# Optimization experiments

Hardware: AMD Instinct MI355X
Metric: run time of the kernel (lower is better)

## Reference

```python
import jax, jax.numpy as jnp
import numpy as np

B, T, DU, DM, DA, DF = 8, 2048, 512, 512, 256, 12
L_STAGES = 4   # number of routing stages
R_ITERS = 1    # diversity refinement iterations in selector
GAMMA = 1.0    # coverage_gamma
EPS = 1e-6
SCALE = float(np.sqrt(DA))


def setup_inputs() -> dict:
    key = jax.random.key(0)
    ks = jax.random.split(key, 16)
    w = lambda k, shape, fan_in: (jax.random.normal(k, shape, jnp.float32) / np.sqrt(fan_in)).astype(jnp.float32)
    return {
        'u': jax.random.normal(ks[0], (B, T, DU), jnp.float32),
        'structural_features': jax.random.normal(ks[1], (B, T, DF), jnp.float32),
        'similarity': jax.random.uniform(ks[2], (B, T, T), jnp.float32),
        'memory0': jax.random.normal(ks[3], (B, DM), jnp.float32),
        'Wq': w(ks[4], (DA, DM), DM),
        'Wk': w(ks[5], (DA, DU), DU),
        'Wv': w(ks[6], (DU, DU), DU),
        'sb_w1': w(ks[7], (DA, 3), 3),
        'sb_b1': jnp.zeros((DA,), jnp.float32),
        'sb_w2': w(ks[8], (1, DA), DA),
        'sb_b2': jnp.zeros((1,), jnp.float32),
        'log_temp': jnp.zeros((), jnp.float32),
        'W_ih': w(ks[9], (3 * DM, DU + 4), DU + 4),
        'b_ih': jnp.zeros((3 * DM,), jnp.float32),
        'W_hh': w(ks[10], (3 * DM, DM), DM),
        'b_hh': jnp.zeros((3 * DM,), jnp.float32),
    }


def _selection_stats(y, u):
    # y: [B,T], u: [B,T,DU] -> c: [B,4]
    Tn = u.shape[1]
    y_sum = jnp.maximum(y.sum(axis=1), EPS)                      # [B]
    coverage = y.sum(axis=1) / Tn
    y_norm = y / y_sum[:, None]
    entropy = -(y_norm * jnp.log(jnp.maximum(y_norm, EPS))).sum(axis=1)
    centroid = jnp.einsum('bt,btd->bd', y, u)                    # unnormalized [B,DU]
    cen = centroid / y_sum[:, None]
    dist = jnp.linalg.norm(u - cen[:, None, :], axis=-1)         # [B,T]
    spread = (y * dist).sum(axis=1) / y_sum
    wsq = (y * jnp.sum(u * u, axis=-1)).sum(axis=1)              # [B]
    csq = jnp.sum(centroid * centroid, axis=1)
    compact = 2.0 * (y_sum * wsq - csq) / jnp.maximum(y_sum * y_sum, EPS)
    return jnp.stack([coverage, entropy, spread, compact], axis=1)


def reference(u, structural_features, similarity, memory0, Wq, Wk, Wv,
              sb_w1, sb_b1, sb_w2, sb_b2, log_temp, W_ih, b_ih, W_hh, b_hh):
    k = jnp.einsum('btu,au->bta', u, Wk)                         # [B,T,DA]
    v = jnp.einsum('btu,vu->btv', u, Wv)                         # [B,T,DU]
    desc = structural_features[..., -4:-1]                       # [B,T,3]
    sbias = (jax.nn.gelu(desc @ sb_w1.T + sb_b1, approximate=False) @ sb_w2.T + sb_b2)[..., 0]
    temp = jnp.clip(jnp.exp(log_temp), 0.1, 10.0)
    memory = memory0
    prev = None
    outs = []
    for _ in range(L_STAGES):
        q = memory @ Wq.T                                        # [B,DA]
        scores = jnp.einsum('bta,ba->bt', k, q) / SCALE + sbias
        if prev is not None:
            scores = scores - GAMMA * jnp.einsum('bts,bs->bt', similarity, prev)
        logits = scores / temp
        y = jax.nn.softmax(logits, axis=1)
        for _r in range(R_ITERS):
            overlap = jnp.einsum('bts,bs->bt', similarity, y)
            penalty = overlap / jnp.maximum(jnp.max(overlap, axis=1, keepdims=True), EPS)
            logits = logits - penalty
            y = jax.nn.softmax(logits, axis=1)
        z = jnp.einsum('bt,btd->bd', y, v)                       # stage token [B,DU]
        c = _selection_stats(y, u)                               # [B,4]
        x = jnp.concatenate([z, c], axis=-1)
        gi = x @ W_ih.T + b_ih
        gh = memory @ W_hh.T + b_hh
        gir, giz, gin = jnp.split(gi, 3, axis=-1)
        ghr, ghz, ghn = jnp.split(gh, 3, axis=-1)
        rg = jax.nn.sigmoid(gir + ghr)
        zg = jax.nn.sigmoid(giz + ghz)
        ng = jnp.tanh(gin + rg * ghn)
        memory = (1.0 - zg) * ng + zg * memory                   # GRUCell update
        prev = y if prev is None else prev + y
        outs.append(z)
    return jnp.stack(outs, axis=1)                               # [B,L,DU]
```

## Files before the change

### kernel.cpp

```cpp
#include <hip/hip_runtime.h>
#include <math.h>

constexpr int cB = 8, cT = 2048, cDU = 512, cDM = 512, cDA = 256, cDF = 12, cL = 4;
constexpr float cEPS = 1e-6f;
constexpr float cSCALE = 16.0f;
constexpr float cGAMMA = 1.0f;

typedef unsigned short u16;
typedef unsigned char u8;
typedef u16 u16x8 __attribute__((ext_vector_type(8)));

constexpr size_t F_SB = 0;
constexpr size_t F_UN = F_SB + 16384;
constexpr size_t F_LG = F_UN + 16384;
constexpr size_t F_Y  = F_LG + 16384;
constexpr size_t F_PR = F_Y  + 16384;
constexpr size_t F_OV = F_PR + 16384;
constexpr size_t F_SP = F_OV + 16384;
constexpr size_t F_QK = F_SP + 256;
constexpr size_t F_M0 = F_QK + 4096;
constexpr size_t F_M1 = F_M0 + 4096;
constexpr size_t F_C  = F_M1 + 4096;
constexpr size_t F_Z  = F_C  + 4096;
constexpr size_t F_SC = F_Z  + 4096;
constexpr size_t F_END = F_SC + 64;
constexpr size_t U_OFFB   = F_END * 4;
constexpr size_t U_BYTES  = (size_t)cB * cT * cDU * 2;
constexpr size_t S8_OFFB  = U_OFFB + U_BYTES;
constexpr size_t S8_BYTES = (size_t)cB * cT * cT;
constexpr size_t WS_NEED_U   = S8_OFFB;
constexpr size_t WS_NEED_ALL = S8_OFFB + S8_BYTES;

__device__ __forceinline__ float wave_sum(float v) {
#pragma unroll
  for (int o = 32; o; o >>= 1) v += __shfl_down(v, o);
  return v;
}
__device__ __forceinline__ u16 f2bf(float f) {
  unsigned u = __float_as_uint(f);
  return (u16)((u + 0x7fffu + ((u >> 16) & 1u)) >> 16);
}
__device__ __forceinline__ float bf2f(u16 h) { return __uint_as_float(((unsigned)h) << 16); }
__device__ __forceinline__ float dot4(float4 a, float4 b) {
  return a.x * b.x + a.y * b.y + a.z * b.z + a.w * b.w;
}
__device__ __forceinline__ unsigned pack4(float a, float b, float c, float d) {
  unsigned b0 = (unsigned)(a * 255.f + 0.5f);
  unsigned b1 = (unsigned)(b * 255.f + 0.5f);
  unsigned b2 = (unsigned)(c * 255.f + 0.5f);
  unsigned b3 = (unsigned)(d * 255.f + 0.5f);
  return b0 | (b1 << 8) | (b2 << 16) | (b3 << 24);
}
__device__ __forceinline__ void dotu8(float& sd, unsigned w, float4 p) {
  sd += (float)(w & 255u) * p.x + (float)((w >> 8) & 255u) * p.y +
        (float)((w >> 16) & 255u) * p.z + (float)(w >> 24) * p.w;
}

__global__ __launch_bounds__(256) void k_init(
    const float* __restrict__ u, const float* __restrict__ sf,
    const float* __restrict__ mem0,
    const float* __restrict__ w1, const float* __restrict__ b1,
    const float* __restrict__ w2, const float* __restrict__ b2,
    float* __restrict__ wsf, u16* __restrict__ ubf, int use_ubf) {
  const int tid = threadIdx.x;
  const int gt = blockIdx.x * 256 + tid;
  const int nt = gridDim.x * 256;
  const int wv = tid >> 6, lane = tid & 63;
  const int gw = blockIdx.x * 4 + wv;
  const int nw = gridDim.x * 4;

  for (int i = gt; i < cB * cDM; i += nt) wsf[F_M0 + i] = mem0[i];

  if (use_ubf) {
    const int NU8 = cB * cT * cDU / 8;
    const float4* src = (const float4*)u;
    for (int c = gt; c < NU8; c += nt) {
      float4 f0 = src[(size_t)c * 2], f1 = src[(size_t)c * 2 + 1];
      u16x8 o;
      o[0] = f2bf(f0.x); o[1] = f2bf(f0.y); o[2] = f2bf(f0.z); o[3] = f2bf(f0.w);
      o[4] = f2bf(f1.x); o[5] = f2bf(f1.y); o[6] = f2bf(f1.z); o[7] = f2bf(f1.w);
      *(u16x8*)(ubf + (size_t)c * 8) = o;
    }
  }
  for (int row = gw; row < cB * cT; row += nw) {
    float d0 = sf[(size_t)row * cDF + 8];
    float d1 = sf[(size_t)row * cDF + 9];
    float d2 = sf[(size_t)row * cDF + 10];
    float acc = 0.f;
#pragma unroll
    for (int i = 0; i < 4; ++i) {
      int a = lane * 4 + i;
      float h = d0 * w1[a * 3 + 0] + d1 * w1[a * 3 + 1] + d2 * w1[a * 3 + 2] + b1[a];
      float g = 0.5f * h * (1.0f + erff(h * 0.70710678118654752f));
      acc += g * w2[a];
    }
    float un = 0.f;
    const float4* ur = (const float4*)(u + (size_t)row * cDU);
#pragma unroll
    for (int m = 0; m < 2; ++m) { float4 x = ur[lane + m * 64]; un += dot4(x, x); }
    acc = wave_sum(acc);
    un = wave_sum(un);
    if (lane == 0) { wsf[F_SB + row] = acc + b2[0]; wsf[F_UN + row] = un; }
  }
}

__global__ __launch_bounds__(1024) void k_qqk(const float* __restrict__ mem,
                                              const float* __restrict__ Wq,
                                              const float* __restrict__ Wk,
                                              float* __restrict__ qk,
                                              float* __restrict__ c_raw) {
  __shared__ float qs[cDA];
  __shared__ float red2[1024];
  int b = blockIdx.x, tid = threadIdx.x;
  int wv = tid >> 6, lane = tid & 63;
  if (tid < cDU) c_raw[b * cDU + tid] = 0.f;
  const float4* mr = (const float4*)(mem + (size_t)b * cDM);
  float4 m0 = mr[lane * 2], m1 = mr[lane * 2 + 1];
#pragma unroll
  for (int ii = 0; ii < 16; ++ii) {
    int a = wv * 16 + ii;
    const float4* wr = (const float4*)(Wq + (size_t)a * cDM);
    float acc = dot4(m0, wr[lane * 2]) + dot4(m1, wr[lane * 2 + 1]);
    acc = wave_sum(acc);
    if (lane == 0) qs[a] = acc;
  }
  __syncthreads();
  int j = tid & 511;
  int half = tid >> 9;
  float acc = 0.f;
#pragma unroll 4
  for (int a = half * 128; a < half * 128 + 128; ++a)
    acc += Wk[(size_t)a * cDU + j] * qs[a];
  red2[tid] = acc;
  __syncthreads();
  if (tid < 512) qk[b * cDU + j] = red2[tid] + red2[tid + 512];
}

__global__ __launch_bounds__(256) void k_scores(
    const u16* __restrict__ ubf, const float* __restrict__ uf,
    const float* __restrict__ qk, const float* __restrict__ sbias,
    const u8* __restrict__ sim8, const float* __restrict__ simf,
    const float* __restrict__ prev, const float* __restrict__ log_temp,
    float gamma, int use_ubf, int use_s8, float* __restrict__ logits) {
  int wid = (blockIdx.x * blockDim.x + threadIdx.x) >> 6;
  int lane = threadIdx.x & 63;
  int b = wid >> 11;
  const float4* qk4 = (const float4*)(qk + (size_t)b * cDU);
  float4 q0 = qk4[lane * 2], q1 = qk4[lane * 2 + 1];
  float acc;
  if (use_ubf) {
    u16x8 s = *(const u16x8*)(ubf + (size_t)wid * cDU + lane * 8);
    acc = bf2f(s[0]) * q0.x + bf2f(s[1]) * q0.y + bf2f(s[2]) * q0.z + bf2f(s[3]) * q0.w +
          bf2f(s[4]) * q1.x + bf2f(s[5]) * q1.y + bf2f(s[6]) * q1.z + bf2f(s[7]) * q1.w;
  } else {
    const float4* ur = (const float4*)(uf + (size_t)wid * cDU);
    acc = dot4(ur[lane * 2], q0) + dot4(ur[lane * 2 + 1], q1);
  }
  acc *= (1.0f / cSCALE);
  if (gamma != 0.0f) {
    float sd = 0.f;
    const float4* pr4 = (const float4*)(prev + (size_t)b * cT);
    if (use_s8) {
#pragma unroll
      for (int m = 0; m < 2; ++m) {
        uint4 sq = *(const uint4*)(sim8 + (size_t)wid * cT + m * 1024 + lane * 16);
        const float4* pb = pr4 + m * 256 + lane * 4;
        dotu8(sd, sq.x, pb[0]); dotu8(sd, sq.y, pb[1]);
        dotu8(sd, sq.z, pb[2]); dotu8(sd, sq.w, pb[3]);
      }
      sd *= (1.0f / 255.0f);
    } else {
      const float4* sr = (const float4*)(simf + (size_t)wid * cT);
#pragma unroll
      for (int m = 0; m < 8; ++m) sd += dot4(sr[lane + m * 64], pr4[lane + m * 64]);
    }
    acc -= gamma * sd;
  }
  acc = wave_sum(acc);
  if (lane == 0) {
    float temp = fminf(fmaxf(expf(log_temp[0]), 0.1f), 10.0f);
    logits[wid] = (acc + sbias[wid]) / temp;
  }
}

__global__ __launch_bounds__(256) void k_overlap(
    const u8* __restrict__ sim8c, u8* __restrict__ sim8w,
    const float* __restrict__ simf,
    const float* __restrict__ logits, int use_s8, int convert,
    float* __restrict__ overlap) {
  __shared__ float ylds[2176];
  __shared__ float red[256];
  const int tid = threadIdx.x;
  const int wv = tid >> 6, lane = tid & 63;
  const int b = blockIdx.x >> 9;
  float l[8];
  float mx = -INFINITY;
#pragma unroll
  for (int e = 0; e < 8; ++e) { l[e] = logits[b * cT + e * 256 + tid]; mx = fmaxf(mx, l[e]); }
  red[tid] = mx; __syncthreads();
  for (int s2 = 128; s2; s2 >>= 1) { if (tid < s2) red[tid] = fmaxf(red[tid], red[tid + s2]); __syncthreads(); }
  mx = red[0]; __syncthreads();
  float sum = 0.f;
#pragma unroll
  for (int e = 0; e < 8; ++e) {
    float ev = expf(l[e] - mx);
    sum += ev;
    int s = e * 256 + tid;
    ylds[s + (s >> 4)] = ev;
  }
  red[tid] = sum; __syncthreads();
  for (int s2 = 128; s2; s2 >>= 1) { if (tid < s2) red[tid] += red[tid + s2]; __syncthreads(); }
  float invS = 1.f / red[0];
  __syncthreads();
  int row = blockIdx.x * 4 + wv;
  float acc = 0.f;
  if (use_s8 && !convert) {
#pragma unroll
    for (int m = 0; m < 2; ++m) {
      uint4 sq = *(const uint4*)(sim8c + (size_t)row * cT + m * 1024 + lane * 16);
      int s0 = m * 1024 + lane * 16;
#pragma unroll
      for (int k = 0; k < 4; ++k) {
        unsigned w = (&sq.x)[k];
        int s = s0 + k * 4;
        acc += (float)(w & 255u)         * ylds[s + (s >> 4)] +
               (float)((w >> 8) & 255u)  * ylds[(s + 1) + ((s + 1) >> 4)] +
               (float)((w >> 16) & 255u) * ylds[(s + 2) + ((s + 2) >> 4)] +
               (float)(w >> 24)          * ylds[(s + 3) + ((s + 3) >> 4)];
      }
    }
    acc *= (1.0f / 255.0f);
  } else {
#pragma unroll
    for (int m = 0; m < 2; ++m) {
      const float4* sr = (const float4*)(simf + (size_t)row * cT + m * 1024 + lane * 16);
      uint4 oq;
#pragma unroll
      for (int k = 0; k < 4; ++k) {
        float4 sv = sr[k];
        int s = m * 1024 + lane * 16 + k * 4;
        acc += sv.x * ylds[s + (s >> 4)] + sv.y * ylds[(s + 1) + ((s + 1) >> 4)] +
               sv.z * ylds[(s + 2) + ((s + 2) >> 4)] + sv.w * ylds[(s + 3) + ((s + 3) >> 4)];
        (&oq.x)[k] = pack4(sv.x, sv.y, sv.z, sv.w);
      }
      if (convert)
        *(uint4*)(sim8w + (size_t)row * cT + m * 1024 + lane * 16) = oq;
    }
  }
  acc = wave_sum(acc);
  if (lane == 0) overlap[row] = acc * invS;
}

__global__ __launch_bounds__(256) void k_statcen(
    const float* __restrict__ overlap, const float* __restrict__ logits,
    const float* __restrict__ unorm2,
    const u16* __restrict__ ubf, const float* __restrict__ uf, int use_ubf,
    float* __restrict__ y, float* __restrict__ prev,
    float* __restrict__ scal, float* __restrict__ c_raw, int first_stage) {
  __shared__ float ylds[2048];
  __shared__ float comb[2048];
  __shared__ float red[256];
  const int tid = threadIdx.x;
  const int wv = tid >> 6, lane = tid & 63;
  const int ch = blockIdx.x, b = blockIdx.y;
  float o[8], l[8], yv[8];
  float mo = -INFINITY;
#pragma unroll
  for (int e = 0; e < 8; ++e) { o[e] = overlap[b * cT + e * 256 + tid]; mo = fmaxf(mo, o[e]); }
  red[tid] = mo; __syncthreads();
  for (int s2 = 128; s2; s2 >>= 1) { if (tid < s2) red[tid] = fmaxf(red[tid], red[tid + s2]); __syncthreads(); }
  mo = fmaxf(red[0], cEPS); __syncthreads();
  float ml = -INFINITY;
#pragma unroll
  for (int e = 0; e < 8; ++e) { l[e] = logits[b * cT + e * 256 + tid] - o[e] / mo; ml = fmaxf(ml, l[e]); }
  red[tid] = ml; __syncthreads();
  for (int s2 = 128; s2; s2 >>= 1) { if (tid < s2) red[tid] = fmaxf(red[tid], red[tid + s2]); __syncthreads(); }
  ml = red[0]; __syncthreads();
  float sum = 0.f;
#pragma unroll
  for (int e = 0; e < 8; ++e) { l[e] = expf(l[e] - ml); sum += l[e]; }
  red[tid] = sum; __syncthreads();
  for (int s2 = 128; s2; s2 >>= 1) { if (tid < s2) red[tid] += red[tid + s2]; __syncthreads(); }
  float inv = 1.f / red[0]; __syncthreads();
  float ysr_p = 0.f, wsq_p = 0.f;
#pragma unroll
  for (int e = 0; e < 8; ++e) {
    yv[e] = l[e] * inv;
    ylds[e * 256 + tid] = yv[e];
    ysr_p += yv[e];
    wsq_p += yv[e] * unorm2[b * cT + e * 256 + tid];
  }
  red[tid] = ysr_p; __syncthreads();
  for (int s2 = 128; s2; s2 >>= 1) { if (tid < s2) red[tid] += red[tid + s2]; __syncthreads(); }
  float ysr = red[0]; __syncthreads();
  float ysc = fmaxf(ysr, cEPS);
  red[tid] = wsq_p; __syncthreads();
  for (int s2 = 128; s2; s2 >>= 1) { if (tid < s2) red[tid] += red[tid + s2]; __syncthreads(); }
  float wsq = red[0]; __syncthreads();
  float ent_p = 0.f;
#pragma unroll
  for (int e = 0; e < 8; ++e) {
    float yn = yv[e] / ysc;
    ent_p -= yn * logf(fmaxf(yn, cEPS));
  }
  red[tid] = ent_p; __syncthreads();
  for (int s2 = 128; s2; s2 >>= 1) { if (tid < s2) red[tid] += red[tid + s2]; __syncthreads(); }
  float ent = red[0]; __syncthreads();
  if (ch == 0) {
#pragma unroll
    for (int e = 0; e < 8; ++e) {
      int idx = b * cT + e * 256 + tid;
      y[idx] = yv[e];
      if (first_stage) prev[idx] = yv[e]; else prev[idx] += yv[e];
    }
    if (tid == 0) {
      scal[b * 8 + 0] = ysc;
      scal[b * 8 + 1] = ysr / (float)cT;
      scal[b * 8 + 2] = ent;
      scal[b * 8 + 3] = wsq;
    }
  }
  float acc[8] = {};
  for (int i = 0; i < 16; ++i) {
    int r = ch * 64 + wv * 16 + i;
    float yvv = ylds[r];
    int row = b * cT + r;
    if (use_ubf) {
      u16x8 s8 = *(const u16x8*)(ubf + (size_t)row * cDU + lane * 8);
#pragma unroll
      for (int e = 0; e < 8; ++e) acc[e] += yvv * bf2f(s8[e]);
    } else {
      const float4* ur = (const float4*)(uf + (size_t)row * cDU);
      float4 a0 = ur[lane * 2], a1 = ur[lane * 2 + 1];
      acc[0] += yvv * a0.x; acc[1] += yvv * a0.y; acc[2] += yvv * a0.z; acc[3] += yvv * a0.w;
      acc[4] += yvv * a1.x; acc[5] += yvv * a1.y; acc[6] += yvv * a1.z; acc[7] += yvv * a1.w;
    }
  }
  __syncthreads();
#pragma unroll
  for (int e = 0; e < 8; ++e) comb[wv * 512 + lane * 8 + e] = acc[e];
  __syncthreads();
  float s0 = comb[tid] + comb[512 + tid] + comb[1024 + tid] + comb[1536 + tid];
  float s1 = comb[tid + 256] + comb[512 + tid + 256] + comb[1024 + tid + 256] + comb[1536 + tid + 256];
  atomicAdd(&c_raw[b * cDU + tid], s0);
  atomicAdd(&c_raw[b * cDU + tid + 256], s1);
}

__global__ __launch_bounds__(256) void k_zyd(
    const float* __restrict__ c_raw, const float* __restrict__ Wv,
    const u16* __restrict__ ubf, const float* __restrict__ uf, int use_ubf,
    const float* __restrict__ unorm2, const float* __restrict__ y,
    float* __restrict__ z, float* __restrict__ scal, float* __restrict__ sprp) {
  __shared__ float s4[4];
  int wv = threadIdx.x >> 6, lane = threadIdx.x & 63;
  if (blockIdx.x < 1024) {
    int wid = blockIdx.x * 4 + wv;
    int b = wid >> 9, j = wid & 511;
    const float4* c4 = (const float4*)(c_raw + (size_t)b * cDU);
    const float4* w4 = (const float4*)(Wv + (size_t)j * cDU);
    float acc = dot4(c4[lane * 2], w4[lane * 2]) + dot4(c4[lane * 2 + 1], w4[lane * 2 + 1]);
    acc = wave_sum(acc);
    if (lane == 0) z[b * cDU + j] = acc;
    return;
  }
  int unit = blockIdx.x - 1024;
  int b = unit >> 5, tc = unit & 31;
  float ysc = scal[b * 8 + 0];
  float inv = 1.f / ysc;
  const float4* c4 = (const float4*)(c_raw + (size_t)b * cDU);
  float4 cr0 = c4[lane * 2], cr1 = c4[lane * 2 + 1];
  float4 cx0, cx1;
  cx0.x = cr0.x * inv; cx0.y = cr0.y * inv; cx0.z = cr0.z * inv; cx0.w = cr0.w * inv;
  cx1.x = cr1.x * inv; cx1.y = cr1.y * inv; cx1.z = cr1.z * inv; cx1.w = cr1.w * inv;
  float cen2 = wave_sum(dot4(cx0, cx0) + dot4(cx1, cx1));
  if (tc == 0 && wv == 0) {
    float csq = wave_sum(dot4(cr0, cr0) + dot4(cr1, cr1));
    if (lane == 0) scal[b * 8 + 6] = csq;
  }
  float part = 0.f;
  for (int i = 0; i < 16; ++i) {
    int row = b * cT + tc * 64 + wv * 16 + i;
    float dot;
    if (use_ubf) {
      u16x8 s = *(const u16x8*)(ubf + (size_t)row * cDU + lane * 8);
      dot = bf2f(s[0]) * cx0.x + bf2f(s[1]) * cx0.y + bf2f(s[2]) * cx0.z + bf2f(s[3]) * cx0.w +
            bf2f(s[4]) * cx1.x + bf2f(s[5]) * cx1.y + bf2f(s[6]) * cx1.z + bf2f(s[7]) * cx1.w;
    } else {
      const float4* ur = (const float4*)(uf + (size_t)row * cDU);
      dot = dot4(ur[lane * 2], cx0) + dot4(ur[lane * 2 + 1], cx1);
    }
    dot = wave_sum(dot);
    if (lane == 0) {
      float d2 = unorm2[row] - 2.f * dot + cen2;
      part += y[row] * sqrtf(fmaxf(d2, 0.f));
    }
  }
  if (lane == 0) s4[wv] = part;
  __syncthreads();
  if (threadIdx.x == 0) sprp[b * 32 + tc] = s4[0] + s4[1] + s4[2] + s4[3];
}

__global__ __launch_bounds__(256) void k_gru(const float* __restrict__ z,
                                             const float* __restrict__ scal,
                                             const float* __restrict__ sprp,
                                             const float* __restrict__ memin,
                                             float* __restrict__ memout,
                                             const float* __restrict__ W_ih,
                                             const float* __restrict__ b_ih,
                                             const float* __restrict__ W_hh,
                                             const float* __restrict__ b_hh,
                                             float* __restrict__ out, int stage) {
  int wid = blockIdx.x * 4 + (threadIdx.x >> 6);
  int lane = threadIdx.x & 63;
  int b = wid >> 9, i = wid & 511;
  const float4* xz = (const float4*)(z + (size_t)b * cDU);
  const float4* xm = (const float4*)(memin + (size_t)b * cDM);
  float4 z0 = xz[lane * 2], z1 = xz[lane * 2 + 1];
  float4 m0 = xm[lane * 2], m1 = xm[lane * 2 + 1];
  float ysc = scal[b * 8 + 0];
  float sv = (lane < 32) ? sprp[b * 32 + lane] : 0.f;
  float spr_raw = wave_sum(sv);
  float aI[3], aH[3];
#pragma unroll
  for (int g = 0; g < 3; ++g) {
    size_t row = (size_t)(g * 512 + i);
    const float4* wI = (const float4*)(W_ih + row * 516);
    float a = dot4(z0, wI[lane * 2]) + dot4(z1, wI[lane * 2 + 1]);
    if (lane == 0) {
      float4 wt = wI[128];
      float cov = scal[b * 8 + 1], ent = scal[b * 8 + 2];
      float spr = spr_raw / ysc;
      float cmp = 2.f * (ysc * scal[b * 8 + 3] - scal[b * 8 + 6]) / fmaxf(ysc * ysc, cEPS);
      a += cov * wt.x + ent * wt.y + spr * wt.z + cmp * wt.w;
    }
    aI[g] = wave_sum(a);
    const float4* wH = (const float4*)(W_hh + row * cDM);
    float h = dot4(m0, wH[lane * 2]) + dot4(m1, wH[lane * 2 + 1]);
    aH[g] = wave_sum(h);
  }
  if (lane == 0) {
    float gir = aI[0] + b_ih[i],        ghr = aH[0] + b_hh[i];
    float giz = aI[1] + b_ih[512 + i],  ghz = aH[1] + b_hh[512 + i];
    float gin = aI[2] + b_ih[1024 + i], ghn = aH[2] + b_hh[1024 + i];
    float rg = 1.f / (1.f + expf(-(gir + ghr)));
    float zg = 1.f / (1.f + expf(-(giz + ghz)));
    float ng = tanhf(gin + rg * ghn);
    float mold = memin[b * cDM + i];
    memout[b * cDM + i] = (1.f - zg) * ng + zg * mold;
    out[(size_t)(b * cL + stage) * cDU + i] = z[b * cDU + i];
  }
}

extern "C" void kernel_launch(void* const* d_in, const int* in_sizes, int n_in,
                              void* d_out, int out_size, void* d_ws, size_t ws_size,
                              hipStream_t stream) {
  const float* u    = (const float*)d_in[0];
  const float* sf   = (const float*)d_in[1];
  const float* sim  = (const float*)d_in[2];
  const float* mem0 = (const float*)d_in[3];
  const float* Wq   = (const float*)d_in[4];
  const float* Wk   = (const float*)d_in[5];
  const float* Wv   = (const float*)d_in[6];
  const float* sbw1 = (const float*)d_in[7];
  const float* sbb1 = (const float*)d_in[8];
  const float* sbw2 = (const float*)d_in[9];
  const float* sbb2 = (const float*)d_in[10];
  const float* logt = (const float*)d_in[11];
  const float* W_ih = (const float*)d_in[12];
  const float* b_ih = (const float*)d_in[13];
  const float* W_hh = (const float*)d_in[14];
  const float* b_hh = (const float*)d_in[15];
  float* out = (float*)d_out;
  float* ws  = (float*)d_ws;
  u16* ubf  = (u16*)((char*)d_ws + U_OFFB);
  u8* sim8  = (u8*)((char*)d_ws + S8_OFFB);

  const int use_ubf = (ws_size >= WS_NEED_U) ? 1 : 0;
  const int use_s8  = (ws_size >= WS_NEED_ALL) ? 1 : 0;

  k_init<<<1024, 256, 0, stream>>>(u, sf, mem0, sbw1, sbb1, sbw2, sbb2,
                                   ws, ubf, use_ubf);

  for (int stage = 0; stage < cL; ++stage) {
    float* mcur = ws + ((stage & 1) ? F_M1 : F_M0);
    float* mnxt = ws + ((stage & 1) ? F_M0 : F_M1);
    k_qqk<<<cB, 1024, 0, stream>>>(mcur, Wq, Wk, ws + F_QK, ws + F_C);
    k_scores<<<4096, 256, 0, stream>>>(ubf, u, ws + F_QK, ws + F_SB, sim8, sim,
                                       ws + F_PR, logt, stage == 0 ? 0.0f : cGAMMA,
                                       use_ubf, use_s8, ws + F_LG);
    k_overlap<<<4096, 256, 0, stream>>>(sim8, sim8, sim, ws + F_LG, use_s8,
                                        (stage == 0 && use_s8) ? 1 : 0, ws + F_OV);
    k_statcen<<<dim3(32, cB), 256, 0, stream>>>(ws + F_OV, ws + F_LG, ws + F_UN,
                                                ubf, u, use_ubf,
                                                ws + F_Y, ws + F_PR, ws + F_SC, ws + F_C,
                                                stage == 0 ? 1 : 0);
    k_zyd<<<1280, 256, 0, stream>>>(ws + F_C, Wv, ubf, u, use_ubf,
                                    ws + F_UN, ws + F_Y, ws + F_Z, ws + F_SC, ws + F_SP);
    k_gru<<<1024, 256, 0, stream>>>(ws + F_Z, ws + F_SC, ws + F_SP, mcur, mnxt,
                                    W_ih, b_ih, W_hh, b_hh, out, stage);
  }
}
```

Baseline: 568.4 us.

## Precompute Wk^T·Wq once and coarsen overlap kernel to four rows per wave

The product A = Wk^T Wq (512x512) is computed once in extra blocks of the init kernel, so each stage's query projection becomes a single matrix-vector product over A. This replaces the old 8-block kernel that ran two dependent matvecs per stage with low parallelism. Separately, the overlap kernel now has each wave handle four similarity rows, which cuts the grid from 4096 to 1024 blocks and spreads the per-block softmax recomputation over more rows. The cost is a one-time 512x512x256 GEMM, 1 MB of extra workspace, and some change in floating-point summation order.

```diff
diff --git a/kernel.cpp b/kernel.cpp
--- a/kernel.cpp
+++ b/kernel.cpp
@@ -23,7 +23,8 @@
 constexpr size_t F_C  = F_M1 + 4096;
 constexpr size_t F_Z  = F_C  + 4096;
 constexpr size_t F_SC = F_Z  + 4096;
-constexpr size_t F_END = F_SC + 64;
+constexpr size_t F_A  = F_SC + 64;
+constexpr size_t F_END = F_A + 262144;
 constexpr size_t U_OFFB   = F_END * 4;
 constexpr size_t U_BYTES  = (size_t)cB * cT * cDU * 2;
 constexpr size_t S8_OFFB  = U_OFFB + U_BYTES;
@@ -59,15 +60,42 @@
 __global__ __launch_bounds__(256) void k_init(
     const float* __restrict__ u, const float* __restrict__ sf,
     const float* __restrict__ mem0,
+    const float* __restrict__ Wq, const float* __restrict__ Wk,
     const float* __restrict__ w1, const float* __restrict__ b1,
     const float* __restrict__ w2, const float* __restrict__ b2,
     float* __restrict__ wsf, u16* __restrict__ ubf, int use_ubf) {
   const int tid = threadIdx.x;
+  if (blockIdx.x >= 1024) {
+    __shared__ float wkj[32][8];
+    int j0 = (blockIdx.x - 1024) * 8;
+    float acc[8][2] = {};
+    for (int a0 = 0; a0 < cDA; a0 += 32) {
+      wkj[tid >> 3][tid & 7] = Wk[(size_t)(a0 + (tid >> 3)) * cDU + j0 + (tid & 7)];
+      __syncthreads();
+#pragma unroll 8
+      for (int aa = 0; aa < 32; ++aa) {
+        float wq0 = Wq[(size_t)(a0 + aa) * cDM + tid * 2];
+        float wq1 = Wq[(size_t)(a0 + aa) * cDM + tid * 2 + 1];
+#pragma unroll
+        for (int r = 0; r < 8; ++r) {
+          acc[r][0] += wkj[aa][r] * wq0;
+          acc[r][1] += wkj[aa][r] * wq1;
+        }
+      }
+      __syncthreads();
+    }
+#pragma unroll
+    for (int r = 0; r < 8; ++r) {
+      wsf[F_A + (size_t)(j0 + r) * cDU + tid * 2] = acc[r][0];
+      wsf[F_A + (size_t)(j0 + r) * cDU + tid * 2 + 1] = acc[r][1];
+    }
+    return;
+  }
   const int gt = blockIdx.x * 256 + tid;
-  const int nt = gridDim.x * 256;
+  const int nt = 1024 * 256;
   const int wv = tid >> 6, lane = tid & 63;
   const int gw = blockIdx.x * 4 + wv;
-  const int nw = gridDim.x * 4;
+  const int nw = 1024 * 4;
 
   for (int i = gt; i < cB * cDM; i += nt) wsf[F_M0 + i] = mem0[i];
 
@@ -104,36 +132,20 @@
   }
 }
 
-__global__ __launch_bounds__(1024) void k_qqk(const float* __restrict__ mem,
-                                              const float* __restrict__ Wq,
-                                              const float* __restrict__ Wk,
-                                              float* __restrict__ qk,
-                                              float* __restrict__ c_raw) {
-  __shared__ float qs[cDA];
-  __shared__ float red2[1024];
-  int b = blockIdx.x, tid = threadIdx.x;
-  int wv = tid >> 6, lane = tid & 63;
-  if (tid < cDU) c_raw[b * cDU + tid] = 0.f;
+__global__ __launch_bounds__(256) void k_qk(const float* __restrict__ A,
+                                            const float* __restrict__ mem,
+                                            float* __restrict__ qk,
+                                            float* __restrict__ c_raw) {
+  int wv = threadIdx.x >> 6, lane = threadIdx.x & 63;
+  int wid = blockIdx.x * 4 + wv;
+  int b = wid >> 9, j = wid & 511;
+  const float4* ar = (const float4*)(A + (size_t)j * cDM);
   const float4* mr = (const float4*)(mem + (size_t)b * cDM);
-  float4 m0 = mr[lane * 2], m1 = mr[lane * 2 + 1];
-#pragma unroll
-  for (int ii = 0; ii < 16; ++ii) {
-    int a = wv * 16 + ii;
-    const float4* wr = (const float4*)(Wq + (size_t)a * cDM);
-    float acc = dot4(m0, wr[lane * 2]) + dot4(m1, wr[lane * 2 + 1]);
-    acc = wave_sum(acc);
-    if (lane == 0) qs[a] = acc;
-  }
-  __syncthreads();
-  int j = tid & 511;
-  int half = tid >> 9;
-  float acc = 0.f;
-#pragma unroll 4
-  for (int a = half * 128; a < half * 128 + 128; ++a)
-    acc += Wk[(size_t)a * cDU + j] * qs[a];
-  red2[tid] = acc;
-  __syncthreads();
-  if (tid < 512) qk[b * cDU + j] = red2[tid] + red2[tid + 512];
+  float acc = dot4(ar[lane * 2], mr[lane * 2]) + dot4(ar[lane * 2 + 1], mr[lane * 2 + 1]);
+  acc = wave_sum(acc);
+  if (lane == 0) qk[b * cDU + j] = acc;
+  int gt = blockIdx.x * 256 + threadIdx.x;
+  if (gt < cB * cDU) c_raw[gt] = 0.f;
 }
 
 __global__ __launch_bounds__(256) void k_scores(
@@ -192,7 +204,7 @@
   __shared__ float red[256];
   const int tid = threadIdx.x;
   const int wv = tid >> 6, lane = tid & 63;
-  const int b = blockIdx.x >> 9;
+  const int b = blockIdx.x >> 7;
   float l[8];
   float mx = -INFINITY;
 #pragma unroll
@@ -212,43 +224,45 @@
   for (int s2 = 128; s2; s2 >>= 1) { if (tid < s2) red[tid] += red[tid + s2]; __syncthreads(); }
   float invS = 1.f / red[0];
   __syncthreads();
-  int row = blockIdx.x * 4 + wv;
-  float acc = 0.f;
-  if (use_s8 && !convert) {
-#pragma unroll
-    for (int m = 0; m < 2; ++m) {
-      uint4 sq = *(const uint4*)(sim8c + (size_t)row * cT + m * 1024 + lane * 16);
-      int s0 = m * 1024 + lane * 16;
-#pragma unroll
-      for (int k = 0; k < 4; ++k) {
-        unsigned w = (&sq.x)[k];
-        int s = s0 + k * 4;
-        acc += (float)(w & 255u)         * ylds[s + (s >> 4)] +
-               (float)((w >> 8) & 255u)  * ylds[(s + 1) + ((s + 1) >> 4)] +
-               (float)((w >> 16) & 255u) * ylds[(s + 2) + ((s + 2) >> 4)] +
-               (float)(w >> 24)          * ylds[(s + 3) + ((s + 3) >> 4)];
+  for (int r = 0; r < 4; ++r) {
+    int row = blockIdx.x * 16 + wv * 4 + r;
+    float acc = 0.f;
+    if (use_s8 && !convert) {
+#pragma unroll
+      for (int m = 0; m < 2; ++m) {
+        uint4 sq = *(const uint4*)(sim8c + (size_t)row * cT + m * 1024 + lane * 16);
+        int s0 = m * 1024 + lane * 16;
+#pragma unroll
+        for (int k = 0; k < 4; ++k) {
+          unsigned w = (&sq.x)[k];
+          int s = s0 + k * 4;
+          acc += (float)(w & 255u)         * ylds[s + (s >> 4)] +
+                 (float)((w >> 8) & 255u)  * ylds[(s + 1) + ((s + 1) >> 4)] +
+                 (float)((w >> 16) & 255u) * ylds[(s + 2) + ((s + 2) >> 4)] +
+                 (float)(w >> 24)          * ylds[(s + 3) + ((s + 3) >> 4)];
+        }
       }
-    }
-    acc *= (1.0f / 255.0f);
-  } else {
-#pragma unroll
-    for (int m = 0; m < 2; ++m) {
-      const float4* sr = (const float4*)(simf + (size_t)row * cT + m * 1024 + lane * 16);
-      uint4 oq;
-#pragma unroll
-      for (int k = 0; k < 4; ++k) {
-        float4 sv = sr[k];
-        int s = m * 1024 + lane * 16 + k * 4;
-        acc += sv.x * ylds[s + (s >> 4)] + sv.y * ylds[(s + 1) + ((s + 1) >> 4)] +
-               sv.z * ylds[(s + 2) + ((s + 2) >> 4)] + sv.w * ylds[(s + 3) + ((s + 3) >> 4)];
-        (&oq.x)[k] = pack4(sv.x, sv.y, sv.z, sv.w);
+      acc *= (1.0f / 255.0f);
+    } else {
+#pragma unroll
+      for (int m = 0; m < 2; ++m) {
+        const float4* sr = (const float4*)(simf + (size_t)row * cT + m * 1024 + lane * 16);
+        uint4 oq;
+#pragma unroll
+        for (int k = 0; k < 4; ++k) {
+          float4 sv = sr[k];
+          int s = m * 1024 + lane * 16 + k * 4;
+          acc += sv.x * ylds[s + (s >> 4)] + sv.y * ylds[(s + 1) + ((s + 1) >> 4)] +
+                 sv.z * ylds[(s + 2) + ((s + 2) >> 4)] + sv.w * ylds[(s + 3) + ((s + 3) >> 4)];
+          (&oq.x)[k] = pack4(sv.x, sv.y, sv.z, sv.w);
+        }
+        if (convert)
+          *(uint4*)(sim8w + (size_t)row * cT + m * 1024 + lane * 16) = oq;
       }
-      if (convert)
-        *(uint4*)(sim8w + (size_t)row * cT + m * 1024 + lane * 16) = oq;
-    }
-  }
-  acc = wave_sum(acc);
-  if (lane == 0) overlap[row] = acc * invS;
+    }
+    acc = wave_sum(acc);
+    if (lane == 0) overlap[row] = acc * invS;
+  }
 }
 
 __global__ __launch_bounds__(256) void k_statcen(
@@ -478,17 +492,17 @@
   const int use_ubf = (ws_size >= WS_NEED_U) ? 1 : 0;
   const int use_s8  = (ws_size >= WS_NEED_ALL) ? 1 : 0;
 
-  k_init<<<1024, 256, 0, stream>>>(u, sf, mem0, sbw1, sbb1, sbw2, sbb2,
+  k_init<<<1088, 256, 0, stream>>>(u, sf, mem0, Wq, Wk, sbw1, sbb1, sbw2, sbb2,
                                    ws, ubf, use_ubf);
 
   for (int stage = 0; stage < cL; ++stage) {
     float* mcur = ws + ((stage & 1) ? F_M1 : F_M0);
     float* mnxt = ws + ((stage & 1) ? F_M0 : F_M1);
-    k_qqk<<<cB, 1024, 0, stream>>>(mcur, Wq, Wk, ws + F_QK, ws + F_C);
+    k_qk<<<1024, 256, 0, stream>>>(ws + F_A, mcur, ws + F_QK, ws + F_C);
     k_scores<<<4096, 256, 0, stream>>>(ubf, u, ws + F_QK, ws + F_SB, sim8, sim,
                                        ws + F_PR, logt, stage == 0 ? 0.0f : cGAMMA,
                                        use_ubf, use_s8, ws + F_LG);
-    k_overlap<<<4096, 256, 0, stream>>>(sim8, sim8, sim, ws + F_LG, use_s8,
+    k_overlap<<<1024, 256, 0, stream>>>(sim8, sim8, sim, ws + F_LG, use_s8,
                                         (stage == 0 && use_s8) ? 1 : 0, ws + F_OV);
     k_statcen<<<dim3(32, cB), 256, 0, stream>>>(ws + F_OV, ws + F_LG, ws + F_UN,
                                                 ubf, u, use_ubf,
```

Result: faster. 502.3 us (-11.6%).
